# Kernel tuning notes

Measured on AMD Instinct MI355X. Metric: run time of the kernel, lower is better.

## Reference

```python
import jax, jax.numpy as jnp
import numpy as np

B, S, D, H, F = 4, 2048, 1024, 16, 4096
HD = D // H
EPS = 1e-4


def setup_inputs() -> dict:
    key = jax.random.key(0)
    ks = jax.random.split(key, 10)
    sd = 1.0 / np.sqrt(D)
    sf = 1.0 / np.sqrt(F)
    return {
        "x":  jax.random.normal(ks[0], (B, S, D), dtype=jnp.float32),
        "wq": jax.random.uniform(ks[1], (D, D), jnp.float32, -sd, sd),
        "wk": jax.random.uniform(ks[2], (D, D), jnp.float32, -sd, sd),
        "wv": jax.random.uniform(ks[3], (D, D), jnp.float32, -sd, sd),
        "wu": jax.random.uniform(ks[4], (D, D), jnp.float32, -sd, sd),
        "bu": jax.random.uniform(ks[5], (D,), jnp.float32, -sd, sd),
        "w1": jax.random.uniform(ks[6], (F, D), jnp.float32, -sd, sd),
        "b1": jax.random.uniform(ks[7], (F,), jnp.float32, -sd, sd),
        "w2": jax.random.uniform(ks[8], (D, F), jnp.float32, -sf, sf),
        "b2": jax.random.uniform(ks[9], (D,), jnp.float32, -sf, sf),
    }


def _ln(x):
    # LN with gamma=1, beta=0 (module initializes them to ones/zeros)
    mean = jnp.mean(x, axis=-1, keepdims=True)
    var = jnp.mean((x - mean) ** 2, axis=-1, keepdims=True)
    return (x - mean) / jnp.sqrt(var + EPS)


def _mhsa(x, wq, wk, wv, wu, bu):
    b, s, d = x.shape
    # torch Linear: y = x @ W.T
    q = (x @ wq.T).reshape(b, s, H, HD).transpose(0, 2, 1, 3)  # bhsd
    k = (x @ wk.T).reshape(b, s, H, HD).transpose(0, 2, 1, 3)
    v = (x @ wv.T).reshape(b, s, H, HD).transpose(0, 2, 1, 3)
    scores = jnp.einsum("bhqd,bhkd->bhqk", q, k) / jnp.sqrt(jnp.float32(HD))
    causal = jnp.triu(jnp.ones((s, s), dtype=bool), k=1)
    scores = jnp.where(causal, -jnp.inf, scores)
    attn = jax.nn.softmax(scores, axis=-1)
    ctx = jnp.einsum("bhqk,bhkd->bhqd", attn, v)
    ctx = ctx.transpose(0, 2, 1, 3).reshape(b, s, d)
    return ctx @ wu.T + bu


def reference(x, wq, wk, wv, wu, bu, w1, b1, w2, b2):
    attn = _mhsa(_ln(x), wq, wk, wv, wu, bu)
    h = x + attn
    ff = jax.nn.relu(_ln(h) @ w1.T + b1) @ w2.T + b2
    return h + ff
```

## Files before the change

kernel.cpp:

```cpp
#include <hip/hip_runtime.h>
#include <hip/hip_bf16.h>
#include <stdint.h>

#define BB   4
#define SS   2048
#define DD   1024
#define NH   16
#define HDIM 64
#define FF   4096
#define NROW (BB*SS)
#define LN_EPS 1e-4f

typedef __attribute__((ext_vector_type(8))) short  bf16x8;
typedef __attribute__((ext_vector_type(4))) float  f32x4;

__device__ __forceinline__ ushort f2bf(float f) {
    uint32_t u = __builtin_bit_cast(uint32_t, f);
    u += 0x7fff + ((u >> 16) & 1);
    return (ushort)(u >> 16);
}

__device__ __forceinline__ void load_lds16(const void* g, void* l) {
    __builtin_amdgcn_global_load_lds(
        (const __attribute__((address_space(1))) void*)g,
        (__attribute__((address_space(3))) void*)l, 16, 0, 0);
}

__global__ __launch_bounds__(256) void cvt_all(
    const float* __restrict__ wq, const float* __restrict__ wk,
    const float* __restrict__ wv, const float* __restrict__ wu,
    const float* __restrict__ w1, const float* __restrict__ w2,
    ushort* __restrict__ wqkv, ushort* __restrict__ wu_b,
    ushort* __restrict__ w1_b, ushort* __restrict__ w2_b) {
    int i = blockIdx.x * 256 + threadIdx.x;
    const float* src; ushort* dst; int off;
    if (i < 262144)       { src = wq; dst = wqkv;           off = i; }
    else if (i < 524288)  { src = wk; dst = wqkv + 1048576; off = i - 262144; }
    else if (i < 786432)  { src = wv; dst = wqkv + 2097152; off = i - 524288; }
    else if (i < 1048576) { src = wu; dst = wu_b;           off = i - 786432; }
    else if (i < 2097152) { src = w1; dst = w1_b;           off = i - 1048576; }
    else                  { src = w2; dst = w2_b;           off = i - 2097152; }
    float4 v = ((const float4*)src)[off];
    ushort4 o;
    o.x = f2bf(v.x); o.y = f2bf(v.y); o.z = f2bf(v.z); o.w = f2bf(v.w);
    ((ushort4*)dst)[off] = o;
}

__global__ __launch_bounds__(256) void ln_kernel(const float* __restrict__ x,
                                                 ushort* __restrict__ out) {
    int row = blockIdx.x;
    const float4* xr = (const float4*)(x + (size_t)row * DD);
    float4 v = xr[threadIdx.x];
    float s  = v.x + v.y + v.z + v.w;
    float ss = v.x*v.x + v.y*v.y + v.z*v.z + v.w*v.w;
    #pragma unroll
    for (int o = 32; o; o >>= 1) {
        s  += __shfl_xor(s, o);
        ss += __shfl_xor(ss, o);
    }
    __shared__ float ps[4], pss[4];
    if ((threadIdx.x & 63) == 0) { ps[threadIdx.x >> 6] = s; pss[threadIdx.x >> 6] = ss; }
    __syncthreads();
    s  = ps[0] + ps[1] + ps[2] + ps[3];
    ss = pss[0] + pss[1] + pss[2] + pss[3];
    float mean = s * (1.0f / DD);
    float var  = ss * (1.0f / DD) - mean * mean;
    float rstd = rsqrtf(var + LN_EPS);
    ushort4 o4;
    o4.x = f2bf((v.x - mean) * rstd);
    o4.y = f2bf((v.y - mean) * rstd);
    o4.z = f2bf((v.z - mean) * rstd);
    o4.w = f2bf((v.w - mean) * rstd);
    ((ushort4*)(out + (size_t)row * DD))[threadIdx.x] = o4;
}

template<int MODE>
__global__ __launch_bounds__(256, 2) void gemm_bt(
    const ushort* __restrict__ A, const ushort* __restrict__ B,
    void* __restrict__ C, const float* __restrict__ bias,
    const float* __restrict__ resid, int M, int N, int K)
{
    __shared__ ushort As[128 * 32];
    __shared__ ushort Bs[128 * 32];

    int nn  = N >> 7;
    int nwg = (M >> 7) * nn;
    int bid = blockIdx.x;
    int wg  = (bid & 7) * (nwg >> 3) + (bid >> 3);
    int tm = wg / nn, tn = wg % nn;
    size_t m0 = (size_t)tm * 128, n0 = (size_t)tn * 128;

    int tid = threadIdx.x, w = tid >> 6, lane = tid & 63;
    int lq = lane & 15, g = lane >> 4;
    int wr = w >> 1, wc = w & 1;

    f32x4 acc[4][4] = {};

    const int f0 = w * 1024 + lane * 8;

    for (int k0 = 0; k0 < K; k0 += 32) {
        __syncthreads();
        #pragma unroll
        for (int i = 0; i < 2; i++) {
            int f = f0 + i * 512;
            int r = f >> 5, c = f & 31;
            load_lds16(A + (m0 + r) * K + k0 + c, As + w * 1024 + i * 512);
            load_lds16(B + (n0 + r) * K + k0 + c, Bs + w * 1024 + i * 512);
        }
        __syncthreads();

        bf16x8 a[4], b[4];
        #pragma unroll
        for (int mt = 0; mt < 4; mt++)
            a[mt] = *(const bf16x8*)&As[(wr * 64 + mt * 16 + lq) * 32 + g * 8];
        #pragma unroll
        for (int nt = 0; nt < 4; nt++)
            b[nt] = *(const bf16x8*)&Bs[(wc * 64 + nt * 16 + lq) * 32 + g * 8];
        #pragma unroll
        for (int mt = 0; mt < 4; mt++)
            #pragma unroll
            for (int nt = 0; nt < 4; nt++)
                acc[mt][nt] = __builtin_amdgcn_mfma_f32_16x16x32_bf16(
                    a[mt], b[nt], acc[mt][nt], 0, 0, 0);
    }

    #pragma unroll
    for (int mt = 0; mt < 4; mt++) {
        #pragma unroll
        for (int nt = 0; nt < 4; nt++) {
            #pragma unroll
            for (int r = 0; r < 4; r++) {
                size_t row = m0 + wr * 64 + mt * 16 + g * 4 + r;
                size_t col = n0 + wc * 64 + nt * 16 + lq;
                float v = acc[mt][nt][r];
                if (MODE == 0) {
                    ((ushort*)C)[row * N + col] = f2bf(v);
                } else if (MODE == 1) {
                    ((float*)C)[row * N + col] = v + bias[col] + resid[row * N + col];
                } else {
                    float t = v + bias[col];
                    ((ushort*)C)[row * N + col] = f2bf(t > 0.f ? t : 0.f);
                }
            }
        }
    }
}

__global__ __launch_bounds__(256) void transpose_v(const ushort* __restrict__ qkv,
                                                   ushort* __restrict__ vt) {
    int idx = blockIdx.x * 256 + threadIdx.x;
    int s   = idx & (SS - 1);
    int cg  = (idx >> 11) & 7;
    int bh  = idx >> 14;
    int b = bh >> 4, h = bh & 15;
    bf16x8 v = *(const bf16x8*)(qkv + ((size_t)b * SS + s) * 3072 + 2048 + h * 64 + cg * 8);
    #pragma unroll
    for (int j = 0; j < 8; j++)
        vt[((size_t)bh * 64 + cg * 8 + j) * SS + s] = ((ushort*)&v)[j];
}

__global__ __launch_bounds__(256, 3) void attn_kernel(const ushort* __restrict__ qkv,
                                                      const ushort* __restrict__ vt,
                                                      ushort* __restrict__ ctx) {
    __shared__ ushort   Kl[2][64 * 64];
    __shared__ ushort   Vl[2][64 * 64];
    __shared__ uint32_t Pl[4][32 * 20];

    int pr = blockIdx.x;
    int bh = blockIdx.y;
    int b = bh >> 4, h = bh & 15;
    int tid = threadIdx.x, wid = tid >> 6, lane = tid & 63;
    int lq = lane & 15, g = lane >> 4;
    int sr = tid >> 3;
    int sc = (tid & 7) * 8;
    const float CE = 0.125f * 1.44269504f;

    const ushort* kbase = qkv + (size_t)b * SS * 3072 + 1024 + h * 64;
    const ushort* vbase = vt + (size_t)bh * 64 * SS;

    #define LOADSTAGE(T) do { int k0_ = (T) * 64;                                   \
        kr0 = *(const bf16x8*)(kbase + (size_t)(k0_ + sr) * 3072 + sc);             \
        kr1 = *(const bf16x8*)(kbase + (size_t)(k0_ + 32 + sr) * 3072 + sc);        \
        vr0 = *(const bf16x8*)(vbase + (size_t)sr * SS + k0_ + sc);                 \
        vr1 = *(const bf16x8*)(vbase + (size_t)(32 + sr) * SS + k0_ + sc); } while (0)

    #define WRITESTAGE(BUF) do {                                                    \
        int r0_ = sr, r1_ = 32 + sr, cc_ = sc >> 3;                                 \
        *(bf16x8*)&Kl[BUF][r0_ * 64 + ((cc_ ^ (r0_ & 7)) << 3)] = kr0;              \
        *(bf16x8*)&Kl[BUF][r1_ * 64 + ((cc_ ^ (r1_ & 7)) << 3)] = kr1;              \
        *(bf16x8*)&Vl[BUF][r0_ * 64 + ((cc_ ^ (r0_ & 7)) << 3)] = vr0;              \
        *(bf16x8*)&Vl[BUF][r1_ * 64 + ((cc_ ^ (r1_ & 7)) << 3)] = vr1; } while (0)

    #pragma unroll 1
    for (int half = 0; half < 2; half++) {
        int bx = half ? (31 - pr) : pr;
        int q0 = bx * 64;
        int qrow = q0 + wid * 16 + lq;
        const size_t qoff = ((size_t)b * SS + qrow) * 3072 + h * 64;
        bf16x8 qf0 = *(const bf16x8*)(qkv + qoff + g * 8);
        bf16x8 qf1 = *(const bf16x8*)(qkv + qoff + 32 + g * 8);

        f32x4 oacc[4] = {};
        float m = -1e30f, l = 0.f;
        int ntile = bx + 1;

        bf16x8 kr0, kr1, vr0, vr1;
        LOADSTAGE(0);
        __syncthreads();
        WRITESTAGE(0);
        int cur = 0;

        #pragma unroll 1
        for (int t = 0; t < ntile; ++t) {
            __syncthreads();
            if (t + 1 < ntile) LOADSTAGE(t + 1);

            f32x4 sa[4];
            __builtin_amdgcn_s_setprio(1);
            #pragma unroll
            for (int mt = 0; mt < 4; mt++) {
                int row = mt * 16 + lq;
                sa[mt] = f32x4{0.f, 0.f, 0.f, 0.f};
                bf16x8 a0 = *(const bf16x8*)&Kl[cur][row * 64 + ((g ^ (row & 7)) << 3)];
                sa[mt] = __builtin_amdgcn_mfma_f32_16x16x32_bf16(a0, qf0, sa[mt], 0, 0, 0);
                bf16x8 a1 = *(const bf16x8*)&Kl[cur][row * 64 + (((4 + g) ^ (row & 7)) << 3)];
                sa[mt] = __builtin_amdgcn_mfma_f32_16x16x32_bf16(a1, qf1, sa[mt], 0, 0, 0);
            }
            __builtin_amdgcn_s_setprio(0);

            float p[4][4];
            float tmax = -1e30f;
            if (t == ntile - 1) {
                int k0 = t * 64;
                #pragma unroll
                for (int mt = 0; mt < 4; mt++)
                    #pragma unroll
                    for (int r = 0; r < 4; r++) {
                        float s = sa[mt][r];
                        int key = k0 + mt * 16 + g * 4 + r;
                        if (key > qrow) s = -1e30f;
                        p[mt][r] = s;
                        tmax = fmaxf(tmax, s);
                    }
            } else {
                #pragma unroll
                for (int mt = 0; mt < 4; mt++)
                    #pragma unroll
                    for (int r = 0; r < 4; r++) {
                        float s = sa[mt][r];
                        p[mt][r] = s;
                        tmax = fmaxf(tmax, s);
                    }
            }
            tmax = fmaxf(tmax, __shfl_xor(tmax, 16));
            tmax = fmaxf(tmax, __shfl_xor(tmax, 32));
            float mnew  = fmaxf(m, tmax);
            float alpha = exp2f((m - mnew) * CE);
            float sum = 0.f;
            #pragma unroll
            for (int mt = 0; mt < 4; mt++)
                #pragma unroll
                for (int r = 0; r < 4; r++) {
                    float e = exp2f((p[mt][r] - mnew) * CE);
                    p[mt][r] = e;
                    sum += e;
                }
            sum += __shfl_xor(sum, 16);
            sum += __shfl_xor(sum, 32);
            l = l * alpha + sum;
            m = mnew;
            #pragma unroll
            for (int mt = 0; mt < 4; mt++)
                #pragma unroll
                for (int r = 0; r < 4; r++) oacc[mt][r] *= alpha;

            #pragma unroll
            for (int mt = 0; mt < 4; mt++)
                #pragma unroll
                for (int w2 = 0; w2 < 2; w2++) {
                    uint32_t pk = (uint32_t)f2bf(p[mt][2 * w2]) |
                                  ((uint32_t)f2bf(p[mt][2 * w2 + 1]) << 16);
                    Pl[wid][(mt * 8 + g * 2 + w2) * 20 + lq] = pk;
                }

            __builtin_amdgcn_s_setprio(1);
            #pragma unroll
            for (int ks = 0; ks < 2; ks++) {
                union { uint32_t w[4]; bf16x8 v; } pb;
                #pragma unroll
                for (int c = 0; c < 4; c++)
                    pb.w[c] = Pl[wid][(ks * 16 + g * 4 + c) * 20 + lq];
                #pragma unroll
                for (int mt = 0; mt < 4; mt++) {
                    int row = mt * 16 + lq;
                    bf16x8 af = *(const bf16x8*)&Vl[cur][row * 64 + (((ks * 4 + g) ^ (row & 7)) << 3)];
                    oacc[mt] = __builtin_amdgcn_mfma_f32_16x16x32_bf16(af, pb.v, oacc[mt], 0, 0, 0);
                }
            }
            __builtin_amdgcn_s_setprio(0);

            if (t + 1 < ntile) WRITESTAGE(cur ^ 1);
            cur ^= 1;
        }

        float inv = 1.f / l;
        ushort* cb = ctx + ((size_t)b * SS + qrow) * DD + h * 64;
        #pragma unroll
        for (int mt = 0; mt < 4; mt++)
            #pragma unroll
            for (int r = 0; r < 4; r++)
                cb[mt * 16 + g * 4 + r] = f2bf(oacc[mt][r] * inv);
    }
    #undef LOADSTAGE
    #undef WRITESTAGE
}

extern "C" void kernel_launch(void* const* d_in, const int* in_sizes, int n_in,
                              void* d_out, int out_size, void* d_ws, size_t ws_size,
                              hipStream_t stream) {
    const float* x  = (const float*)d_in[0];
    const float* wq = (const float*)d_in[1];
    const float* wk = (const float*)d_in[2];
    const float* wv = (const float*)d_in[3];
    const float* wu = (const float*)d_in[4];
    const float* bu = (const float*)d_in[5];
    const float* w1 = (const float*)d_in[6];
    const float* b1 = (const float*)d_in[7];
    const float* w2 = (const float*)d_in[8];
    const float* b2 = (const float*)d_in[9];
    float* out = (float*)d_out;

    ushort* ws = (ushort*)d_ws;
    size_t off = 0;
    ushort* wqkv = ws + off; off += (size_t)3072 * 1024;
    ushort* wu_b = ws + off; off += (size_t)1024 * 1024;
    ushort* w1_b = ws + off; off += (size_t)4096 * 1024;
    ushort* w2_b = ws + off; off += (size_t)4096 * 1024;
    ushort* lnb  = ws + off; off += (size_t)NROW * DD;
    float*  hbuf = (float*)(ws + off); off += (size_t)NROW * DD * 2;
    ushort* qkv  = ws + off;
    ushort* ctx  = qkv + (size_t)NROW * 3072;
    ushort* gbuf = qkv;
    off += (size_t)NROW * FF;
    ushort* vtb  = ws + off; off += (size_t)NROW * DD;
    (void)ws_size; (void)n_in; (void)in_sizes; (void)out_size;

    cvt_all<<<12288, 256, 0, stream>>>(wq, wk, wv, wu, w1, w2,
                                       wqkv, wu_b, w1_b, w2_b);

    ln_kernel<<<NROW, 256, 0, stream>>>(x, lnb);
    gemm_bt<0><<<(NROW / 128) * (3072 / 128), 256, 0, stream>>>(
        lnb, wqkv, qkv, nullptr, nullptr, NROW, 3072, 1024);
    transpose_v<<<4096, 256, 0, stream>>>(qkv, vtb);
    attn_kernel<<<dim3(16, BB * NH), 256, 0, stream>>>(qkv, vtb, ctx);
    gemm_bt<1><<<(NROW / 128) * (1024 / 128), 256, 0, stream>>>(
        ctx, wu_b, hbuf, bu, x, NROW, 1024, 1024);
    ln_kernel<<<NROW, 256, 0, stream>>>(hbuf, lnb);
    gemm_bt<2><<<(NROW / 128) * (4096 / 128), 256, 0, stream>>>(
        lnb, w1_b, gbuf, b1, nullptr, NROW, 4096, 1024);
    gemm_bt<1><<<(NROW / 128) * (1024 / 128), 256, 0, stream>>>(
        gbuf, w2_b, out, b2, hbuf, NROW, 1024, 4096);
}
```

Measured before the change: 517.5 us.

## Add 256x256-tile 8-wave GEMM with interleaved staging for QKV and FFN1

Adds a 512-thread GEMM kernel computing 256x256 output tiles with double-buffered LDS staged through global_load_lds, XOR-swizzled LDS layout, block-index remapping for L2 locality, and loads for the next K-step interleaved with MFMA phases using barriers and setprio. It replaces the 128x128 GEMM for the QKV projection and the first FFN layer. Larger tiles raise arithmetic intensity and cut global traffic per FLOP. In exchange it uses more registers and LDS (128KB), which lowers occupancy and can leave fewer workgroups for wave balance on the N=3072 case.

Result: no change. 516.6 us (-0.2%).

```diff
diff --git a/kernel.cpp b/kernel.cpp
--- a/kernel.cpp
+++ b/kernel.cpp
@@ -146,6 +146,147 @@
     }
 }
 
+#define MFMA_BF16 __builtin_amdgcn_mfma_f32_16x16x32_bf16
+
+template<int MODE>
+__global__ __launch_bounds__(512, 2) void gemm256(
+    const ushort* __restrict__ Aw, const ushort* __restrict__ Bw,
+    void* __restrict__ C, const float* __restrict__ bias,
+    int M, int N, int K)
+{
+    __shared__ ushort Ls[2][4][8192];
+
+    int nn  = N >> 8;
+    int nwg = (M >> 8) * nn;
+    int bid = blockIdx.x;
+    int wg  = (bid & 7) * (nwg >> 3) + (bid >> 3);
+    int tm = wg / nn, tn = wg % nn;
+    size_t m0 = (size_t)tm * 256, n0 = (size_t)tn * 256;
+
+    int tid = threadIdx.x, wid = tid >> 6, lane = tid & 63;
+    int lq = lane & 15, g = lane >> 4;
+    int wr = wid >> 2, wc = wid & 3;
+
+    f32x4 acc[8][4] = {};
+
+#define STG(Tn, h, dbuf) do {                                                   \
+    int ks_ = (h) >> 1;                                                         \
+    const ushort* s_ = ((h) & 1) ? (Bw + n0 * (size_t)K) : (Aw + m0 * (size_t)K); \
+    int kk_ = (Tn) * 64 + ks_ * 32;                                             \
+    { int F_ = tid;       int r_ = F_ >> 2, c_ = F_ & 3;                        \
+      load_lds16(s_ + (size_t)r_ * K + kk_ + ((c_ ^ ((r_ >> 1) & 3)) * 8),      \
+                 &Ls[dbuf][h][(wid * 64) * 8]); }                               \
+    { int F_ = 512 + tid; int r_ = F_ >> 2, c_ = F_ & 3;                        \
+      load_lds16(s_ + (size_t)r_ * K + kk_ + ((c_ ^ ((r_ >> 1) & 3)) * 8),      \
+                 &Ls[dbuf][h][(512 + wid * 64) * 8]); }                         \
+  } while (0)
+
+#define RD_A(mt, ks) (*(const bf16x8*)&Ls[cur][(ks)*2][((wr*128 + (mt)*16 + lq) * 32) + ((g ^ (((wr*128 + (mt)*16 + lq) >> 1) & 3)) * 8)])
+#define RD_B(nt, ks) (*(const bf16x8*)&Ls[cur][(ks)*2+1][((wc*64 + (nt)*16 + lq) * 32) + ((g ^ (((wc*64 + (nt)*16 + lq) >> 1) & 3)) * 8)])
+
+    STG(0, 0, 0); STG(0, 1, 0); STG(0, 2, 0); STG(0, 3, 0);
+    asm volatile("s_waitcnt vmcnt(4)" ::: "memory");
+    __builtin_amdgcn_sched_barrier(0);
+    __builtin_amdgcn_s_barrier();
+
+    int KT = K >> 6;
+    #pragma unroll 1
+    for (int T = 0; T < KT; ++T) {
+        int cur = T & 1;
+        bool st = (T + 1 < KT);
+        bf16x8 aF[8], bF[4];
+
+        #pragma unroll
+        for (int mt = 0; mt < 8; mt++) aF[mt] = RD_A(mt, 0);
+        bF[0] = RD_B(0, 0); bF[1] = RD_B(1, 0);
+        if (st) STG(T + 1, 0, cur ^ 1);
+        __builtin_amdgcn_s_barrier();
+        asm volatile("s_waitcnt lgkmcnt(0)" ::: "memory");
+        __builtin_amdgcn_sched_barrier(0);
+        __builtin_amdgcn_s_setprio(1);
+        #pragma unroll
+        for (int mt = 0; mt < 8; mt++) {
+            acc[mt][0] = MFMA_BF16(aF[mt], bF[0], acc[mt][0], 0, 0, 0);
+            acc[mt][1] = MFMA_BF16(aF[mt], bF[1], acc[mt][1], 0, 0, 0);
+        }
+        __builtin_amdgcn_s_setprio(0);
+        __builtin_amdgcn_s_barrier();
+
+        bF[2] = RD_B(2, 0); bF[3] = RD_B(3, 0);
+        if (st) STG(T + 1, 1, cur ^ 1);
+        __builtin_amdgcn_s_barrier();
+        asm volatile("s_waitcnt lgkmcnt(0)" ::: "memory");
+        __builtin_amdgcn_sched_barrier(0);
+        __builtin_amdgcn_s_setprio(1);
+        #pragma unroll
+        for (int mt = 0; mt < 8; mt++) {
+            acc[mt][2] = MFMA_BF16(aF[mt], bF[2], acc[mt][2], 0, 0, 0);
+            acc[mt][3] = MFMA_BF16(aF[mt], bF[3], acc[mt][3], 0, 0, 0);
+        }
+        __builtin_amdgcn_s_setprio(0);
+        if (st) asm volatile("s_waitcnt vmcnt(4)" ::: "memory");
+        else    asm volatile("s_waitcnt vmcnt(0)" ::: "memory");
+        __builtin_amdgcn_sched_barrier(0);
+        __builtin_amdgcn_s_barrier();
+
+        #pragma unroll
+        for (int mt = 0; mt < 8; mt++) aF[mt] = RD_A(mt, 1);
+        bF[0] = RD_B(0, 1); bF[1] = RD_B(1, 1);
+        if (st) STG(T + 1, 2, cur ^ 1);
+        __builtin_amdgcn_s_barrier();
+        asm volatile("s_waitcnt lgkmcnt(0)" ::: "memory");
+        __builtin_amdgcn_sched_barrier(0);
+        __builtin_amdgcn_s_setprio(1);
+        #pragma unroll
+        for (int mt = 0; mt < 8; mt++) {
+            acc[mt][0] = MFMA_BF16(aF[mt], bF[0], acc[mt][0], 0, 0, 0);
+            acc[mt][1] = MFMA_BF16(aF[mt], bF[1], acc[mt][1], 0, 0, 0);
+        }
+        __builtin_amdgcn_s_setprio(0);
+        __builtin_amdgcn_s_barrier();
+
+        bF[2] = RD_B(2, 1); bF[3] = RD_B(3, 1);
+        if (st) STG(T + 1, 3, cur ^ 1);
+        __builtin_amdgcn_s_barrier();
+        asm volatile("s_waitcnt lgkmcnt(0)" ::: "memory");
+        __builtin_amdgcn_sched_barrier(0);
+        __builtin_amdgcn_s_setprio(1);
+        #pragma unroll
+        for (int mt = 0; mt < 8; mt++) {
+            acc[mt][2] = MFMA_BF16(aF[mt], bF[2], acc[mt][2], 0, 0, 0);
+            acc[mt][3] = MFMA_BF16(aF[mt], bF[3], acc[mt][3], 0, 0, 0);
+        }
+        __builtin_amdgcn_s_setprio(0);
+        if (st) {
+            asm volatile("s_waitcnt vmcnt(4)" ::: "memory");
+            __builtin_amdgcn_sched_barrier(0);
+        }
+        __builtin_amdgcn_s_barrier();
+    }
+
+    #pragma unroll
+    for (int mt = 0; mt < 8; mt++) {
+        #pragma unroll
+        for (int nt = 0; nt < 4; nt++) {
+            #pragma unroll
+            for (int r = 0; r < 4; r++) {
+                size_t row = m0 + wr * 128 + mt * 16 + g * 4 + r;
+                size_t col = n0 + wc * 64 + nt * 16 + lq;
+                float v = acc[mt][nt][r];
+                if (MODE == 0) {
+                    ((ushort*)C)[row * N + col] = f2bf(v);
+                } else {
+                    float t = v + bias[col];
+                    ((ushort*)C)[row * N + col] = f2bf(t > 0.f ? t : 0.f);
+                }
+            }
+        }
+    }
+#undef STG
+#undef RD_A
+#undef RD_B
+}
+
 __global__ __launch_bounds__(256) void transpose_v(const ushort* __restrict__ qkv,
                                                    ushort* __restrict__ vt) {
     int idx = blockIdx.x * 256 + threadIdx.x;
@@ -349,15 +490,15 @@
                                        wqkv, wu_b, w1_b, w2_b);
 
     ln_kernel<<<NROW, 256, 0, stream>>>(x, lnb);
-    gemm_bt<0><<<(NROW / 128) * (3072 / 128), 256, 0, stream>>>(
-        lnb, wqkv, qkv, nullptr, nullptr, NROW, 3072, 1024);
+    gemm256<0><<<(NROW / 256) * (3072 / 256), 512, 0, stream>>>(
+        lnb, wqkv, qkv, nullptr, NROW, 3072, 1024);
     transpose_v<<<4096, 256, 0, stream>>>(qkv, vtb);
     attn_kernel<<<dim3(16, BB * NH), 256, 0, stream>>>(qkv, vtb, ctx);
     gemm_bt<1><<<(NROW / 128) * (1024 / 128), 256, 0, stream>>>(
         ctx, wu_b, hbuf, bu, x, NROW, 1024, 1024);
     ln_kernel<<<NROW, 256, 0, stream>>>(hbuf, lnb);
-    gemm_bt<2><<<(NROW / 128) * (4096 / 128), 256, 0, stream>>>(
-        lnb, w1_b, gbuf, b1, nullptr, NROW, 4096, 1024);
+    gemm256<2><<<(NROW / 256) * (4096 / 256), 512, 0, stream>>>(
+        lnb, w1_b, gbuf, b1, NROW, 4096, 1024);
     gemm_bt<1><<<(NROW / 128) * (1024 / 128), 256, 0, stream>>>(
         gbuf, w2_b, out, b2, hbuf, NROW, 1024, 4096);
 }
```
